# Kernel optimization log

Hardware: AMD Instinct MI355X
Metric: run time of the kernel (lower is better)

Reference implementation:

```python
import jax, jax.numpy as jnp
import numpy as np

B, D, H, W = 1, 16, 16, 16
C, NH = 528, 8
HD = C // NH      # 66
K = 32            # retrieved memories per token


def setup_inputs() -> dict:
    key = jax.random.key(0)
    ks = jax.random.split(key, 4)
    x = jax.random.normal(ks[0], (B, D, H, W, C), jnp.float32)
    # simulated knn_memory.search output: (B, heads, N, K, 2[k/v], head_dim)
    knn_kv = jax.random.normal(ks[1], (B, NH, D * H * W, K, 2, HD), jnp.float32)
    w_qkv = jax.random.normal(ks[2], (3 * C, C), jnp.float32) * 0.02
    b_qkv = jnp.zeros((3 * C,), jnp.float32)
    w_proj = jax.random.normal(ks[3], (C, C), jnp.float32) * 0.02
    b_proj = jnp.zeros((C,), jnp.float32)
    return {"x": x, "knn_kv": knn_kv, "w_qkv": w_qkv, "b_qkv": b_qkv,
            "w_proj": w_proj, "b_proj": b_proj, "num_heads": NH}


def _l2norm(t):
    # F.normalize(t, dim=-1): t / max(||t||_2, eps)
    n = jnp.linalg.norm(t, axis=-1, keepdims=True)
    return t / jnp.maximum(n, 1e-12)


def _forward(x, knn_kv, w_qkv, b_qkv, w_proj, b_proj, num_heads):
    Bb, Dd, Hh, Ww, Cc = x.shape
    N = Dd * Hh * Ww
    hd = Cc // num_heads
    scaling = hd ** -0.5
    qkv = x.reshape(Bb * N, Cc) @ w_qkv.T + b_qkv
    qkv = qkv.reshape(Bb, N, 3, num_heads, hd).transpose(2, 0, 3, 1, 4)  # (3,B,h,N,hd)
    q, k, v = qkv[0], qkv[1], qkv[2]
    q = _l2norm(q)
    k = _l2norm(k)
    knn_k = knn_kv[..., 0, :]   # (B,h,N,K,hd)
    knn_v = knn_kv[..., 1, :]
    k_comb = jnp.concatenate([knn_k, k[..., None, :]], axis=-2)  # (B,h,N,K+1,hd)
    v_comb = jnp.concatenate([knn_v, v[..., None, :]], axis=-2)
    attn = jnp.einsum('bhnd,bhnkd->bhnk', q, k_comb) * scaling
    attn = jax.nn.softmax(attn, axis=-1)  # stable softmax
    out = jnp.einsum('bhnk,bhnkd->bhnd', attn, v_comb)  # (B,h,N,hd)
    out = out.transpose(0, 2, 1, 3).reshape(Bb * N, num_heads * hd)
    out = out @ w_proj.T + b_proj
    return out.reshape(Bb, Dd, Hh, Ww, Cc)


def reference(x, knn_kv, w_qkv, b_qkv, w_proj, b_proj, num_heads):
    return _forward(x, knn_kv, w_qkv, b_qkv, w_proj, b_proj, num_heads)
```

## Files before the change

### kernel.cpp

```cpp
#include <hip/hip_runtime.h>
#include <hip/hip_bf16.h>
#include <math.h>

#define N_POS 4096
#define C_DIM 528
#define NHEAD 8
#define HDIM  66
#define KNN   32
#define CQKV  1584
#define KP    544
#define NP1   1664
#define NP2   640

typedef __attribute__((ext_vector_type(8))) short short8;
typedef __attribute__((ext_vector_type(4))) float f32x4;
typedef __hip_bfloat16 bf16;

__device__ __forceinline__ short bf16bits(float f) {
    bf16 h = __float2bfloat16(f);
    return *reinterpret_cast<short*>(&h);
}
__device__ __forceinline__ short8 pack8(float4 a, float4 b) {
    short8 r;
    r[0] = bf16bits(a.x); r[1] = bf16bits(a.y);
    r[2] = bf16bits(a.z); r[3] = bf16bits(a.w);
    r[4] = bf16bits(b.x); r[5] = bf16bits(b.y);
    r[6] = bf16bits(b.z); r[7] = bf16bits(b.w);
    return r;
}

template <bool A_F32, bool BF16OUT>
__global__ __launch_bounds__(256) void gemm_fused_kernel(
    const void* __restrict__ Av, int lda,
    const float* __restrict__ B, int Brows,
    const float* __restrict__ bias, void* __restrict__ Cv,
    int Nreal, int ldc, int nbx)
{
    __shared__ short8 As[256];
    __shared__ short8 Bs[256];

    const int tid  = threadIdx.x;
    const int lane = tid & 63;
    const int wid  = tid >> 6;

    const int nwg   = gridDim.x;
    const int chunk = nwg >> 3;
    const int swz   = (blockIdx.x & 7) * chunk + (blockIdx.x >> 3);
    const int bm = (swz / nbx) * 64;
    const int bn = (swz % nbx) * 64;

    const int r0 = tid >> 2;
    const int c0 = tid & 3;
    const int w0 = r0 * 4 + (c0 ^ (r0 & 3));
    const bool bRowOk = (bn + r0) < Brows;

    const int wm = (wid >> 1) * 32;
    const int wn = (wid & 1) * 32;
    const int arow = wm + (lane & 15);
    const int brow = wn + (lane & 15);
    const int apc  = lane >> 4;
    const int aslot = arow * 4 + (apc ^ (arow & 3));
    const int bslot = brow * 4 + (apc ^ (brow & 3));

    auto loadA = [&](int k0) -> short8 {
        const int c = k0 + c0 * 8;
        if constexpr (A_F32) {
            float4 f0 = {0.f,0.f,0.f,0.f}, f1 = {0.f,0.f,0.f,0.f};
            if (c <= C_DIM - 8) {
                const float* ap = (const float*)Av + (size_t)(bm + r0) * lda + c;
                f0 = *(const float4*)ap;
                f1 = *(const float4*)(ap + 4);
            }
            return pack8(f0, f1);
        } else {
            const bf16* ap = (const bf16*)Av + (size_t)(bm + r0) * lda + c;
            return *(const short8*)ap;
        }
    };
    auto loadB = [&](int k0) -> short8 {
        const int c = k0 + c0 * 8;
        float4 f0 = {0.f,0.f,0.f,0.f}, f1 = {0.f,0.f,0.f,0.f};
        if (c <= C_DIM - 8 && bRowOk) {
            const float* bp = B + (size_t)(bn + r0) * C_DIM + c;
            f0 = *(const float4*)bp;
            f1 = *(const float4*)(bp + 4);
        }
        return pack8(f0, f1);
    };

    f32x4 acc[2][2];
    #pragma unroll
    for (int i = 0; i < 2; ++i)
        #pragma unroll
        for (int j = 0; j < 2; ++j)
            acc[i][j] = (f32x4){0.f, 0.f, 0.f, 0.f};

    short8 a0 = loadA(0);
    short8 b0 = loadB(0);

    for (int k0 = 0;; k0 += 32) {
        As[w0] = a0;
        Bs[w0] = b0;
        __syncthreads();
        if (k0 + 32 < KP) {
            a0 = loadA(k0 + 32);
            b0 = loadB(k0 + 32);
        }
        short8 af[2], bfr[2];
        #pragma unroll
        for (int f = 0; f < 2; ++f) af[f]  = As[aslot + f * 64];
        #pragma unroll
        for (int f = 0; f < 2; ++f) bfr[f] = Bs[bslot + f * 64];
        #pragma unroll
        for (int i = 0; i < 2; ++i)
            #pragma unroll
            for (int j = 0; j < 2; ++j)
                acc[i][j] = __builtin_amdgcn_mfma_f32_16x16x32_bf16(
                    af[i], bfr[j], acc[i][j], 0, 0, 0);
        if (k0 + 32 >= KP) break;
        __syncthreads();
    }

    #pragma unroll
    for (int i = 0; i < 2; ++i) {
        const int row = bm + wm + i * 16 + (lane >> 4) * 4;
        #pragma unroll
        for (int j = 0; j < 2; ++j) {
            const int col = bn + wn + j * 16 + (lane & 15);
            if (col < Nreal) {
                const float bv = bias[col];
                #pragma unroll
                for (int rr = 0; rr < 4; ++rr) {
                    const float o = acc[i][j][rr] + bv;
                    if (BF16OUT)
                        ((bf16*)Cv)[(size_t)(row + rr) * ldc + col] = __float2bfloat16(o);
                    else
                        ((float*)Cv)[(size_t)(row + rr) * ldc + col] = o;
                }
            }
        }
    }
}

__global__ __launch_bounds__(256) void attn_kernel(
    const bf16* __restrict__ qkv, const float* __restrict__ knn,
    bf16* __restrict__ out)
{
    const float scaling = 0.12309149097933272f;

    const int bid = blockIdx.x;
    const int tid = threadIdx.x;
    const int g0  = bid << 1;
    const int h   = g0 >> 12;
    const int n0  = g0 & 4095;
    const int n1  = n0 + 1;

    __shared__ float s_knn[2][KNN * 132];
    __shared__ float s_qkv[2][3 * HDIM];
    __shared__ float s_dot[2][KNN + 1];
    __shared__ float s_sc[2][2];

    const float4* kb0 = (const float4*)(knn + (size_t)g0 * (KNN * 132));
    const float4* kb1 = kb0 + KNN * 33;
    float4 r0[4], r1[4];
    float4 e0 = {0.f,0.f,0.f,0.f}, e1 = {0.f,0.f,0.f,0.f};
    #pragma unroll
    for (int i = 0; i < 4; ++i) r0[i] = kb0[tid + 256 * i];
    if (tid < 32) e0 = kb0[1024 + tid];
    #pragma unroll
    for (int i = 0; i < 4; ++i) r1[i] = kb1[tid + 256 * i];
    if (tid < 32) e1 = kb1[1024 + tid];

    const bf16* qp0 = qkv + (size_t)n0 * CQKV + h * HDIM;
    const bf16* qp1 = qp0 + CQKV;
    float qv0 = 0.f, qv1 = 0.f;
    int part = tid / HDIM, d66 = tid - part * HDIM;
    if (tid < 3 * HDIM) {
        qv0 = __bfloat162float(qp0[part * C_DIM + d66]);
        qv1 = __bfloat162float(qp1[part * C_DIM + d66]);
    }

    float4* s40 = (float4*)s_knn[0];
    float4* s41 = (float4*)s_knn[1];
    #pragma unroll
    for (int i = 0; i < 4; ++i) s40[tid + 256 * i] = r0[i];
    if (tid < 32) s40[1024 + tid] = e0;
    #pragma unroll
    for (int i = 0; i < 4; ++i) s41[tid + 256 * i] = r1[i];
    if (tid < 32) s41[1024 + tid] = e1;
    if (tid < 3 * HDIM) {
        s_qkv[0][tid] = qv0;
        s_qkv[1][tid] = qv1;
    }
    __syncthreads();

    const int team  = tid >> 7;
    const int ttid  = tid & 127;
    const int twave = ttid >> 6;
    const int lane  = tid & 63;
    const float* kK = s_knn[team];
    const float* Q  = &s_qkv[team][0];
    const float* KS = &s_qkv[team][HDIM];

    if (twave == 0) {
        const int j = lane >> 1, l2 = lane & 1;
        const float* kr = kK + j * 132;
        float p = 0.f;
        #pragma unroll
        for (int d = 0; d < HDIM / 2; ++d) p += Q[2 * d + l2] * kr[2 * d + l2];
        p += __shfl_xor(p, 1);
        if (l2 == 0) s_dot[team][j] = p;
    } else {
        float aq, ak, qk;
        {
            float qd = Q[lane], kd = KS[lane];
            aq = qd * qd; ak = kd * kd; qk = qd * kd;
            if (lane < 2) {
                float q2 = Q[64 + lane], k2 = KS[64 + lane];
                aq += q2 * q2; ak += k2 * k2; qk += q2 * k2;
            }
        }
        #pragma unroll
        for (int off = 32; off; off >>= 1) {
            aq += __shfl_xor(aq, off);
            ak += __shfl_xor(ak, off);
            qk += __shfl_xor(qk, off);
        }
        if (lane == 0) {
            const float iq = 1.0f / fmaxf(sqrtf(aq), 1e-12f);
            const float ik = 1.0f / fmaxf(sqrtf(ak), 1e-12f);
            s_sc[team][0] = iq * scaling;
            s_sc[team][1] = qk * iq * ik * scaling;
        }
    }
    __syncthreads();

    if (twave == 0) {
        float x = -3.4e38f;
        if (lane < 32)       x = s_dot[team][lane] * s_sc[team][0];
        else if (lane == 32) x = s_sc[team][1];
        float m = x;
        #pragma unroll
        for (int off = 32; off; off >>= 1) m = fmaxf(m, __shfl_xor(m, off));
        float e = (lane < 33) ? expf(x - m) : 0.f;
        float s = e;
        #pragma unroll
        for (int off = 32; off; off >>= 1) s += __shfl_xor(s, off);
        if (lane < 33) s_dot[team][lane] = e / s;
    }
    __syncthreads();

    if (ttid < HDIM) {
        const int d = ttid;
        float acc = s_dot[team][KNN] * s_qkv[team][2 * HDIM + d];
        #pragma unroll 8
        for (int j = 0; j < KNN; ++j)
            acc += s_dot[team][j] * kK[j * 132 + HDIM + d];
        const int n = team ? n1 : n0;
        out[(size_t)n * KP + h * HDIM + d] = __float2bfloat16(acc);
    }
    if (h == 0) {
        if (tid < 16)
            out[(size_t)n0 * KP + C_DIM + tid] = __float2bfloat16(0.f);
        else if (tid < 32)
            out[(size_t)n1 * KP + C_DIM + (tid - 16)] = __float2bfloat16(0.f);
    }
}

extern "C" void kernel_launch(void* const* d_in, const int* in_sizes, int n_in,
                              void* d_out, int out_size, void* d_ws, size_t ws_size,
                              hipStream_t stream)
{
    const float* x      = (const float*)d_in[0];
    const float* knn_kv = (const float*)d_in[1];
    const float* w_qkv  = (const float*)d_in[2];
    const float* b_qkv  = (const float*)d_in[3];
    const float* w_proj = (const float*)d_in[4];
    const float* b_proj = (const float*)d_in[5];
    float* out = (float*)d_out;

    char* ws = (char*)d_ws;
    bf16* qkvb = (bf16*)ws;
    bf16* ab   = (bf16*)(ws + 12976128);

    gemm_fused_kernel<true, true>
        <<<dim3((NP1 / 64) * (N_POS / 64)), 256, 0, stream>>>(
        x, C_DIM, w_qkv, CQKV, b_qkv, qkvb, CQKV, CQKV, NP1 / 64);

    attn_kernel<<<dim3(NHEAD * N_POS / 2), 256, 0, stream>>>(qkvb, knn_kv, ab);

    gemm_fused_kernel<false, false>
        <<<dim3((NP2 / 64) * (N_POS / 64)), 256, 0, stream>>>(
        ab, KP, w_proj, C_DIM, b_proj, out, C_DIM, C_DIM, NP2 / 64);
}
```

Before: 173.8 us.

## Pipeline attention kNN loads with double-buffered direct-to-LDS DMA per wave

The attention kernel is rewritten so that each wave independently processes four (head, position) pairs. The next pair's kNN key/value block is streamed into a second LDS buffer with global_load_lds while the current pair is computed, and the wait uses explicit vmcnt counts. Block-wide __syncthreads phases are replaced by wave-local shuffles, and the launch becomes a smaller persistent-style grid. The large per-wave LDS footprint (about 141KB per block) allows only one block of four waves per CU, so latency hiding depends on the DMA double buffering rather than on occupancy.

Result: slower. 192.0 us (+10.5%).

```diff
diff --git a/kernel.cpp b/kernel.cpp
--- a/kernel.cpp
+++ b/kernel.cpp
@@ -12,9 +12,15 @@
 #define NP1   1664
 #define NP2   640
 
+#define ATTN_BLOCKS  2048
+#define PAIRS_PER_WAVE 4
+
 typedef __attribute__((ext_vector_type(8))) short short8;
 typedef __attribute__((ext_vector_type(4))) float f32x4;
 typedef __hip_bfloat16 bf16;
+
+typedef const __attribute__((address_space(1))) void* gas1;
+typedef __attribute__((address_space(3))) void* las3;
 
 __device__ __forceinline__ short bf16bits(float f) {
     bf16 h = __float2bfloat16(f);
@@ -148,122 +154,134 @@
 {
     const float scaling = 0.12309149097933272f;
 
-    const int bid = blockIdx.x;
-    const int tid = threadIdx.x;
-    const int g0  = bid << 1;
-    const int h   = g0 >> 12;
-    const int n0  = g0 & 4095;
-    const int n1  = n0 + 1;
-
-    __shared__ float s_knn[2][KNN * 132];
-    __shared__ float s_qkv[2][3 * HDIM];
-    __shared__ float s_dot[2][KNN + 1];
-    __shared__ float s_sc[2][2];
-
-    const float4* kb0 = (const float4*)(knn + (size_t)g0 * (KNN * 132));
-    const float4* kb1 = kb0 + KNN * 33;
-    float4 r0[4], r1[4];
-    float4 e0 = {0.f,0.f,0.f,0.f}, e1 = {0.f,0.f,0.f,0.f};
-    #pragma unroll
-    for (int i = 0; i < 4; ++i) r0[i] = kb0[tid + 256 * i];
-    if (tid < 32) e0 = kb0[1024 + tid];
-    #pragma unroll
-    for (int i = 0; i < 4; ++i) r1[i] = kb1[tid + 256 * i];
-    if (tid < 32) e1 = kb1[1024 + tid];
-
-    const bf16* qp0 = qkv + (size_t)n0 * CQKV + h * HDIM;
-    const bf16* qp1 = qp0 + CQKV;
-    float qv0 = 0.f, qv1 = 0.f;
-    int part = tid / HDIM, d66 = tid - part * HDIM;
-    if (tid < 3 * HDIM) {
-        qv0 = __bfloat162float(qp0[part * C_DIM + d66]);
-        qv1 = __bfloat162float(qp1[part * C_DIM + d66]);
-    }
-
-    float4* s40 = (float4*)s_knn[0];
-    float4* s41 = (float4*)s_knn[1];
-    #pragma unroll
-    for (int i = 0; i < 4; ++i) s40[tid + 256 * i] = r0[i];
-    if (tid < 32) s40[1024 + tid] = e0;
-    #pragma unroll
-    for (int i = 0; i < 4; ++i) s41[tid + 256 * i] = r1[i];
-    if (tid < 32) s41[1024 + tid] = e1;
-    if (tid < 3 * HDIM) {
-        s_qkv[0][tid] = qv0;
-        s_qkv[1][tid] = qv1;
-    }
-    __syncthreads();
-
-    const int team  = tid >> 7;
-    const int ttid  = tid & 127;
-    const int twave = ttid >> 6;
-    const int lane  = tid & 63;
-    const float* kK = s_knn[team];
-    const float* Q  = &s_qkv[team][0];
-    const float* KS = &s_qkv[team][HDIM];
-
-    if (twave == 0) {
-        const int j = lane >> 1, l2 = lane & 1;
-        const float* kr = kK + j * 132;
-        float p = 0.f;
-        #pragma unroll
-        for (int d = 0; d < HDIM / 2; ++d) p += Q[2 * d + l2] * kr[2 * d + l2];
-        p += __shfl_xor(p, 1);
-        if (l2 == 0) s_dot[team][j] = p;
-    } else {
-        float aq, ak, qk;
-        {
-            float qd = Q[lane], kd = KS[lane];
-            aq = qd * qd; ak = kd * kd; qk = qd * kd;
-            if (lane < 2) {
-                float q2 = Q[64 + lane], k2 = KS[64 + lane];
-                aq += q2 * q2; ak += k2 * k2; qk += q2 * k2;
-            }
-        }
+    __shared__ float lds[4][2][4422];
+
+    const int tid  = threadIdx.x;
+    const int wv   = tid >> 6;
+    const int lane = tid & 63;
+    const int gbase = (blockIdx.x * 4 + wv) * PAIRS_PER_WAVE;
+
+    float* buf0 = &lds[wv][0][0];
+    float* buf1 = &lds[wv][1][0];
+
+    auto issue_dma = [&](float* dstb, int g) {
+        const char* src = (const char*)(knn + (size_t)g * (KNN * 132));
+        char* dst = (char*)dstb;
+        #pragma unroll
+        for (int i = 0; i < 16; ++i)
+            __builtin_amdgcn_global_load_lds((gas1)(src + i * 1024 + lane * 16),
+                                             (las3)(dst + i * 1024), 16, 0, 0);
+        #pragma unroll
+        for (int t2 = 0; t2 < 2; ++t2)
+            __builtin_amdgcn_global_load_lds((gas1)(src + 16384 + t2 * 256 + lane * 4),
+                                             (las3)(dst + 16384 + t2 * 256), 4, 0, 0);
+    };
+    auto load_qkv = [&](int g, float2& q2, float2& k2, float2& v2) {
+        q2 = {0.f, 0.f}; k2 = {0.f, 0.f}; v2 = {0.f, 0.f};
+        if (lane < 33) {
+            const int n = g & 4095, h = g >> 12;
+            const bf16* qp = qkv + (size_t)n * CQKV + h * HDIM + 2 * lane;
+            const __hip_bfloat162 qb = *(const __hip_bfloat162*)(qp);
+            const __hip_bfloat162 kb = *(const __hip_bfloat162*)(qp + C_DIM);
+            const __hip_bfloat162 vb = *(const __hip_bfloat162*)(qp + 2 * C_DIM);
+            q2.x = __bfloat162float(qb.x); q2.y = __bfloat162float(qb.y);
+            k2.x = __bfloat162float(kb.x); k2.y = __bfloat162float(kb.y);
+            v2.x = __bfloat162float(vb.x); v2.y = __bfloat162float(vb.y);
+        }
+    };
+
+    float2 q2c, k2c, v2c;
+    load_qkv(gbase, q2c, k2c, v2c);
+    issue_dma(buf0, gbase);
+
+    for (int t = 0; t < PAIRS_PER_WAVE; ++t) {
+        float* cur = (t & 1) ? buf1 : buf0;
+        float* nxt = (t & 1) ? buf0 : buf1;
+        const bool hasNext = (t + 1 < PAIRS_PER_WAVE);
+
+        float2 q2n, k2n, v2n;
+        if (hasNext) {
+            load_qkv(gbase + t + 1, q2n, k2n, v2n);
+            issue_dma(nxt, gbase + t + 1);
+            asm volatile("s_waitcnt vmcnt(21)" ::: "memory");
+        } else {
+            asm volatile("s_waitcnt vmcnt(0)" ::: "memory");
+        }
+        __builtin_amdgcn_sched_barrier(0);
+
+        const int g = gbase + t;
+        const int h = g >> 12;
+        const int n = g & 4095;
+
+        float aq = q2c.x * q2c.x + q2c.y * q2c.y;
+        float ak = k2c.x * k2c.x + k2c.y * k2c.y;
+        float qk = q2c.x * k2c.x + q2c.y * k2c.y;
         #pragma unroll
         for (int off = 32; off; off >>= 1) {
             aq += __shfl_xor(aq, off);
             ak += __shfl_xor(ak, off);
             qk += __shfl_xor(qk, off);
         }
-        if (lane == 0) {
-            const float iq = 1.0f / fmaxf(sqrtf(aq), 1e-12f);
-            const float ik = 1.0f / fmaxf(sqrtf(ak), 1e-12f);
-            s_sc[team][0] = iq * scaling;
-            s_sc[team][1] = qk * iq * ik * scaling;
-        }
-    }
-    __syncthreads();
-
-    if (twave == 0) {
-        float x = -3.4e38f;
-        if (lane < 32)       x = s_dot[team][lane] * s_sc[team][0];
-        else if (lane == 32) x = s_sc[team][1];
-        float m = x;
-        #pragma unroll
-        for (int off = 32; off; off >>= 1) m = fmaxf(m, __shfl_xor(m, off));
-        float e = (lane < 33) ? expf(x - m) : 0.f;
-        float s = e;
-        #pragma unroll
-        for (int off = 32; off; off >>= 1) s += __shfl_xor(s, off);
-        if (lane < 33) s_dot[team][lane] = e / s;
-    }
-    __syncthreads();
-
-    if (ttid < HDIM) {
-        const int d = ttid;
-        float acc = s_dot[team][KNN] * s_qkv[team][2 * HDIM + d];
-        #pragma unroll 8
-        for (int j = 0; j < KNN; ++j)
-            acc += s_dot[team][j] * kK[j * 132 + HDIM + d];
-        const int n = team ? n1 : n0;
-        out[(size_t)n * KP + h * HDIM + d] = __float2bfloat16(acc);
-    }
-    if (h == 0) {
-        if (tid < 16)
-            out[(size_t)n0 * KP + C_DIM + tid] = __float2bfloat16(0.f);
-        else if (tid < 32)
-            out[(size_t)n1 * KP + C_DIM + (tid - 16)] = __float2bfloat16(0.f);
+        const float iq = 1.0f / fmaxf(sqrtf(aq), 1e-12f);
+        const float ik = 1.0f / fmaxf(sqrtf(ak), 1e-12f);
+        const float sc0  = iq * scaling;
+        const float slf  = qk * iq * ik * scaling;
+
+        if (lane < 33) {
+            *(float2*)(cur + 4356 + 2 * lane) = q2c;
+            *(float2*)(cur + 32 * 132 + 66 + 2 * lane) = v2c;
+        }
+        asm volatile("s_waitcnt lgkmcnt(0)" ::: "memory");
+        __builtin_amdgcn_sched_barrier(0);
+
+        const int j  = lane >> 1;
+        const int l2 = lane & 1;
+        {
+            const float* kr = cur + j * 132 + l2;
+            const float* Qp = cur + 4356 + l2;
+            float p = 0.f;
+            #pragma unroll
+            for (int d = 0; d < 33; ++d) p += Qp[2 * d] * kr[2 * d];
+            p += __shfl_xor(p, 1);
+            p *= sc0;
+
+            float m = p;
+            #pragma unroll
+            for (int off = 2; off <= 32; off <<= 1) m = fmaxf(m, __shfl_xor(m, off));
+            m = fmaxf(m, slf);
+            const float e = __expf(p - m);
+            float S = e;
+            #pragma unroll
+            for (int off = 2; off <= 32; off <<= 1) S += __shfl_xor(S, off);
+            const float es = __expf(slf - m);
+            const float tot = S + es;
+            float* sp = cur + 32 * 132;
+            if (l2 == 0) sp[j] = e / tot;
+            if (lane == 0) sp[32] = es / tot;
+        }
+        asm volatile("s_waitcnt lgkmcnt(0)" ::: "memory");
+        __builtin_amdgcn_sched_barrier(0);
+
+        if (lane < 33) {
+            const float* sp = cur + 32 * 132;
+            const float* vr = cur + 66 + 2 * lane;
+            float2 acc = {0.f, 0.f};
+            #pragma unroll
+            for (int jj = 0; jj < 33; ++jj) {
+                const float pj = sp[jj];
+                const float2 vj = *(const float2*)(vr + jj * 132);
+                acc.x += pj * vj.x;
+                acc.y += pj * vj.y;
+            }
+            __hip_bfloat162 o2;
+            o2.x = __float2bfloat16(acc.x);
+            o2.y = __float2bfloat16(acc.y);
+            *(__hip_bfloat162*)(out + (size_t)n * KP + h * HDIM + 2 * lane) = o2;
+        } else if (h == 0 && lane < 49) {
+            out[(size_t)n * KP + C_DIM + (lane - 33)] = __float2bfloat16(0.f);
+        }
+
+        q2c = q2n; k2c = k2n; v2c = v2n;
     }
 }
 
@@ -287,7 +305,7 @@
         <<<dim3((NP1 / 64) * (N_POS / 64)), 256, 0, stream>>>(
         x, C_DIM, w_qkv, CQKV, b_qkv, qkvb, CQKV, CQKV, NP1 / 64);
 
-    attn_kernel<<<dim3(NHEAD * N_POS / 2), 256, 0, stream>>>(qkvb, knn_kv, ab);
+    attn_kernel<<<dim3(ATTN_BLOCKS), 256, 0, stream>>>(qkvb, knn_kv, ab);
 
     gemm_fused_kernel<false, false>
         <<<dim3((NP2 / 64) * (N_POS / 64)), 256, 0, stream>>>(
```
